# Kernel optimization log

Measured on AMD Instinct MI355X. Metric: run time of the kernel, lower is better.

The kernel has to match this reference:

```python
import jax, jax.numpy as jnp
import numpy as np

B, D, H, O, E, K = 8192, 1024, 4096, 1024, 8, 2
HG = H // 2  # gate hidden dim


def setup_inputs() -> dict:
    key = jax.random.key(0)
    ks = jax.random.split(key, 6)
    s1 = 1.0 / np.sqrt(D)
    s2 = 1.0 / np.sqrt(H)
    sg = 1.0 / np.sqrt(HG)
    return {
        "x": jax.random.normal(ks[0], (B, D), jnp.float32),
        "W1": jax.random.normal(ks[1], (E, D, H), jnp.float32) * s1,
        "b1": jnp.zeros((E, H), jnp.float32),
        "W2": jax.random.normal(ks[2], (E, H, O), jnp.float32) * s2,
        "b2": jnp.zeros((E, O), jnp.float32),
        "Wg1": jax.random.normal(ks[3], (D, HG), jnp.float32) * s1,
        "bg1": jnp.zeros((HG,), jnp.float32),
        "Wg2": jax.random.normal(ks[4], (HG, E), jnp.float32) * sg,
        "bg2": jnp.zeros((E,), jnp.float32),
    }


def reference(x, W1, b1, W2, b2, Wg1, bg1, Wg2, bg2):
    # Gate: Linear -> ReLU -> Linear -> softmax over experts
    gate_logits = jax.nn.relu(x @ Wg1 + bg1) @ Wg2 + bg2          # [B, E]
    gate_weights = jax.nn.softmax(gate_logits, axis=1)           # [B, E]

    # Top-k selection and renormalization (second softmax, as in torch)
    top_w, top_idx = jax.lax.top_k(gate_weights, K)              # [B, K]
    top_w = jax.nn.softmax(top_w, axis=1)                        # [B, K]

    # Dense per-expert MLPs (the torch code evaluates every expert)
    h = jax.nn.relu(jnp.einsum('bd,edh->beh', x, W1) + b1)       # [B, E, H]
    expert_outputs = jnp.einsum('beh,eho->beo', h, W2) + b2      # [B, E, O]

    # Gather top-k expert outputs and combine with renormalized weights
    gathered = jnp.take_along_axis(expert_outputs, top_idx[:, :, None], axis=1)  # [B, K, O]
    output = jnp.einsum('bk,bko->bo', top_w, gathered)           # [B, O]

    # Load balancing loss (only expert_fractions feeds the loss; the
    # expert_usage loop in the torch code is dead w.r.t. the returned loss)
    expert_fractions = gate_weights.mean(axis=0)                 # [E]
    cv_loss = jnp.sum((expert_fractions - 1.0 / E) ** 2)

    return output, gate_weights, cv_loss
```

## Files before the change

kernel.cpp:

```cpp
#include <hip/hip_runtime.h>

#define B_  8192
#define D_  1024
#define H_  4096
#define O_  1024
#define E_  8
#define HG_ 2048

typedef _Float16 half8 __attribute__((ext_vector_type(8)));
typedef _Float16 half4 __attribute__((ext_vector_type(4)));
typedef float    f32x4 __attribute__((ext_vector_type(4)));

#define MFMA_F16(a, b, c) __builtin_amdgcn_mfma_f32_16x16x32_f16((a), (b), (c), 0, 0, 0)

typedef const unsigned int __attribute__((address_space(1)))* as1_u32;
typedef unsigned int __attribute__((address_space(3)))* as3_u32;

__device__ __forceinline__ void gload_lds16(const void* g, void* s) {
  __builtin_amdgcn_global_load_lds((as1_u32)(g), (as3_u32)(s), 16, 0, 0);
}

__global__ void zero_small(int* cnt, float* colsum) {
  if (threadIdx.x < E_) { cnt[threadIdx.x] = 0; colsum[threadIdx.x] = 0.f; }
}

__global__ void cvt_x(const float* __restrict__ x, _Float16* __restrict__ xh,
                      _Float16* __restrict__ xl) {
  size_t i = ((size_t)blockIdx.x * 256 + threadIdx.x) * 4;
  float4 v = *(const float4*)(x + i);
  _Float16 h0 = (_Float16)v.x, h1 = (_Float16)v.y, h2 = (_Float16)v.z, h3 = (_Float16)v.w;
  half4 hh = {h0, h1, h2, h3};
  half4 ll = {(_Float16)(v.x - (float)h0), (_Float16)(v.y - (float)h1),
              (_Float16)(v.z - (float)h2), (_Float16)(v.w - (float)h3)};
  *(half4*)(xh + i) = hh;
  *(half4*)(xl + i) = ll;
}

template <bool LO>
__global__ void transpose_cvt(const float* __restrict__ in, _Float16* __restrict__ oh,
                              _Float16* __restrict__ ol, int M, int N) {
  __shared__ float t[32][33];
  const size_t boff = (size_t)blockIdx.z * M * N;
  int bx = blockIdx.x * 32, by = blockIdx.y * 32;
  int tx = threadIdx.x, ty = threadIdx.y;
  const float* src = in + boff;
#pragma unroll
  for (int i = ty; i < 32; i += 8) t[i][tx] = src[(size_t)(by + i) * N + bx + tx];
  __syncthreads();
  _Float16* dh = oh + boff;
#pragma unroll
  for (int i = ty; i < 32; i += 8) {
    float v = t[tx][i];
    size_t oidx = (size_t)(bx + i) * M + by + tx;
    _Float16 h = (_Float16)v;
    dh[oidx] = h;
    if (LO) ol[oidx] = (_Float16)(v - (float)h);
  }
}

__global__ __launch_bounds__(256) void gate_gemm(
    const _Float16* __restrict__ xh, const _Float16* __restrict__ xl,
    const _Float16* __restrict__ wh, const _Float16* __restrict__ wl,
    const float* __restrict__ bg1, float* __restrict__ ghid) {
  __shared__ _Float16 sAh[128 * 32], sAl[128 * 32], sBh[128 * 32], sBl[128 * 32];
  const int tid = threadIdx.x, wave = tid >> 6, lane = tid & 63;
  const int m0 = blockIdx.y * 128, n0 = blockIdx.x * 128;
  const int srow = (wave << 4) + (lane >> 2);
  const int scol = (lane & 3) << 3;
  _Float16* dA0 = sAh + (wave * 16) * 32;
  _Float16* dA1 = sAh + (64 + wave * 16) * 32;
  _Float16* dA0l = sAl + (wave * 16) * 32;
  _Float16* dA1l = sAl + (64 + wave * 16) * 32;
  _Float16* dB0 = sBh + (wave * 16) * 32;
  _Float16* dB1 = sBh + (64 + wave * 16) * 32;
  _Float16* dB0l = sBl + (wave * 16) * 32;
  _Float16* dB1l = sBl + (64 + wave * 16) * 32;
  const _Float16* gA0 = xh + (size_t)(m0 + srow) * D_ + scol;
  const _Float16* gA1 = xh + (size_t)(m0 + 64 + srow) * D_ + scol;
  const _Float16* gA0l = xl + (size_t)(m0 + srow) * D_ + scol;
  const _Float16* gA1l = xl + (size_t)(m0 + 64 + srow) * D_ + scol;
  const _Float16* gB0 = wh + (size_t)(n0 + srow) * D_ + scol;
  const _Float16* gB1 = wh + (size_t)(n0 + 64 + srow) * D_ + scol;
  const _Float16* gB0l = wl + (size_t)(n0 + srow) * D_ + scol;
  const _Float16* gB1l = wl + (size_t)(n0 + 64 + srow) * D_ + scol;
  f32x4 acc[4][4] = {};
  const int wm = wave & 1, wn = wave >> 1, fr = lane & 15, fq = lane >> 4;
  for (int k0 = 0; k0 < D_; k0 += 32) {
    __syncthreads();
    gload_lds16(gA0 + k0, dA0);
    gload_lds16(gA1 + k0, dA1);
    gload_lds16(gA0l + k0, dA0l);
    gload_lds16(gA1l + k0, dA1l);
    gload_lds16(gB0 + k0, dB0);
    gload_lds16(gB1 + k0, dB1);
    gload_lds16(gB0l + k0, dB0l);
    gload_lds16(gB1l + k0, dB1l);
    __syncthreads();
    half8 ah[4], al[4], bh[4], bl[4];
#pragma unroll
    for (int i = 0; i < 4; i++) {
      ah[i] = *(const half8*)(sAh + (wm * 64 + i * 16 + fr) * 32 + fq * 8);
      al[i] = *(const half8*)(sAl + (wm * 64 + i * 16 + fr) * 32 + fq * 8);
      bh[i] = *(const half8*)(sBh + (wn * 64 + i * 16 + fr) * 32 + fq * 8);
      bl[i] = *(const half8*)(sBl + (wn * 64 + i * 16 + fr) * 32 + fq * 8);
    }
#pragma unroll
    for (int mi = 0; mi < 4; mi++)
#pragma unroll
      for (int ni = 0; ni < 4; ni++) {
        acc[mi][ni] = MFMA_F16(ah[mi], bh[ni], acc[mi][ni]);
        acc[mi][ni] = MFMA_F16(ah[mi], bl[ni], acc[mi][ni]);
        acc[mi][ni] = MFMA_F16(al[mi], bh[ni], acc[mi][ni]);
      }
  }
#pragma unroll
  for (int mi = 0; mi < 4; mi++)
#pragma unroll
    for (int i = 0; i < 4; i++) {
      int row = m0 + wm * 64 + mi * 16 + fq * 4 + i;
      float* dst = ghid + (size_t)row * HG_ + n0 + wn * 64;
#pragma unroll
      for (int ni = 0; ni < 4; ni++) {
        int col = ni * 16 + fr;
        dst[col] = fmaxf(acc[mi][ni][i] + bg1[n0 + wn * 64 + col], 0.f);
      }
    }
}

__global__ __launch_bounds__(256) void gate_finish(
    const float* __restrict__ ghid, const float* __restrict__ wg2,
    const float* __restrict__ bg2, float* __restrict__ gw, int* __restrict__ tok,
    float* __restrict__ tkw, int* __restrict__ tkf, int* __restrict__ cnt,
    float* __restrict__ colsum) {
  __shared__ int s_e[32];
  __shared__ float s_p[32];
  __shared__ float s_col[E_];
  __shared__ int s_c[E_], s_c2[E_], s_b[E_];
  const int tid = threadIdx.x, wave = tid >> 6, lane = tid & 63;
  if (tid < E_) { s_col[tid] = 0.f; s_c[tid] = 0; s_c2[tid] = 0; }
  __syncthreads();
  for (int it = 0; it < 4; it++) {
    int b = blockIdx.x * 16 + wave * 4 + it;
    const float* g = ghid + (size_t)b * HG_;
    float l[8] = {0, 0, 0, 0, 0, 0, 0, 0};
    for (int j = lane; j < HG_; j += 64) {
      float gv = g[j];
      float4 w0 = *(const float4*)(wg2 + (size_t)j * 8);
      float4 w1 = *(const float4*)(wg2 + (size_t)j * 8 + 4);
      l[0] += gv * w0.x; l[1] += gv * w0.y; l[2] += gv * w0.z; l[3] += gv * w0.w;
      l[4] += gv * w1.x; l[5] += gv * w1.y; l[6] += gv * w1.z; l[7] += gv * w1.w;
    }
#pragma unroll
    for (int off = 32; off; off >>= 1)
#pragma unroll
      for (int r = 0; r < 8; r++) l[r] += __shfl_xor(l[r], off);
    if (lane == 0) {
      float w[8];
      float mx = -1e30f;
#pragma unroll
      for (int r = 0; r < 8; r++) { l[r] += bg2[r]; mx = fmaxf(mx, l[r]); }
      float s = 0.f;
#pragma unroll
      for (int r = 0; r < 8; r++) { w[r] = expf(l[r] - mx); s += w[r]; }
      float inv = 1.f / s;
#pragma unroll
      for (int r = 0; r < 8; r++) w[r] *= inv;
      for (int r = 0; r < 8; r++) {
        gw[(size_t)b * 8 + r] = w[r];
        atomicAdd(&s_col[r], w[r]);
      }
      int i1 = 0;
      for (int r = 1; r < 8; r++) if (w[r] > w[i1]) i1 = r;
      int i2 = (i1 == 0) ? 1 : 0;
      for (int r = 0; r < 8; r++) if (r != i1 && w[r] > w[i2]) i2 = r;
      float e2 = expf(w[i2] - w[i1]);
      float p1 = 1.f / (1.f + e2), p2 = e2 / (1.f + e2);
      int sl = (wave * 4 + it) * 2;
      s_e[sl] = i1; s_p[sl] = p1;
      s_e[sl + 1] = i2; s_p[sl + 1] = p2;
    }
  }
  __syncthreads();
  if (tid < 32) atomicAdd(&s_c[s_e[tid]], 1);
  __syncthreads();
  if (tid < E_) s_b[tid] = atomicAdd(&cnt[tid], s_c[tid]);
  __syncthreads();
  if (tid < 32) {
    int e = s_e[tid];
    int slot = s_b[e] + atomicAdd(&s_c2[e], 1);
    int bb = blockIdx.x * 16 + (tid >> 1);
    tok[e * B_ + slot] = bb;
    tkw[e * B_ + slot] = s_p[tid];
    tkf[e * B_ + slot] = tid & 1;
  }
  if (tid < E_) atomicAdd(&colsum[tid], s_col[tid]);
}

__global__ void prefix_cv(const int* __restrict__ cnt, int* __restrict__ basep,
                          const float* __restrict__ colsum, float* __restrict__ cvout) {
  if (threadIdx.x == 0) {
    int s = 0;
    for (int e = 0; e < E_; e++) { basep[e] = s; s += cnt[e]; }
    float cv = 0.f;
    for (int e = 0; e < E_; e++) {
      float f = colsum[e] * (1.f / B_) - 1.f / E_;
      cv += f * f;
    }
    *cvout = cv;
  }
}

__global__ __launch_bounds__(256) void expert_gemm1(
    const _Float16* __restrict__ xh, const _Float16* __restrict__ w1t,
    const float* __restrict__ b1, const int* __restrict__ tok,
    const int* __restrict__ cnt, const int* __restrict__ basep,
    _Float16* __restrict__ hbuf) {
  const int e = blockIdx.y >> 6, mt = blockIdx.y & 63;
  const int ce = cnt[e];
  if (mt * 128 >= ce) return;
  __shared__ _Float16 sA[128 * 32], sB[128 * 32];
  const int tid = threadIdx.x, wave = tid >> 6, lane = tid & 63;
  const int n0 = blockIdx.x * 128;
  const int srow = (wave << 4) + (lane >> 2), scol = (lane & 3) << 3;
  int r0 = mt * 128 + srow, r1 = r0 + 64;
  if (r0 > ce - 1) r0 = ce - 1;
  if (r1 > ce - 1) r1 = ce - 1;
  const int t0 = tok[e * B_ + r0], t1 = tok[e * B_ + r1];
  const _Float16* gA0 = xh + (size_t)t0 * D_ + scol;
  const _Float16* gA1 = xh + (size_t)t1 * D_ + scol;
  const _Float16* wte = w1t + (size_t)e * H_ * D_;
  const _Float16* gB0 = wte + (size_t)(n0 + srow) * D_ + scol;
  const _Float16* gB1 = wte + (size_t)(n0 + 64 + srow) * D_ + scol;
  _Float16* dA0 = sA + (wave * 16) * 32;
  _Float16* dA1 = sA + (64 + wave * 16) * 32;
  _Float16* dB0 = sB + (wave * 16) * 32;
  _Float16* dB1 = sB + (64 + wave * 16) * 32;
  f32x4 acc[4][4] = {};
  const int wm = wave & 1, wn = wave >> 1, fr = lane & 15, fq = lane >> 4;
  for (int k0 = 0; k0 < D_; k0 += 32) {
    __syncthreads();
    gload_lds16(gA0 + k0, dA0);
    gload_lds16(gA1 + k0, dA1);
    gload_lds16(gB0 + k0, dB0);
    gload_lds16(gB1 + k0, dB1);
    __syncthreads();
    half8 a[4], b[4];
#pragma unroll
    for (int i = 0; i < 4; i++) {
      a[i] = *(const half8*)(sA + (wm * 64 + i * 16 + fr) * 32 + fq * 8);
      b[i] = *(const half8*)(sB + (wn * 64 + i * 16 + fr) * 32 + fq * 8);
    }
#pragma unroll
    for (int mi = 0; mi < 4; mi++)
#pragma unroll
      for (int ni = 0; ni < 4; ni++) acc[mi][ni] = MFMA_F16(a[mi], b[ni], acc[mi][ni]);
  }
  const int base = basep[e];
  float bv[4];
#pragma unroll
  for (int ni = 0; ni < 4; ni++) bv[ni] = b1[e * H_ + n0 + wn * 64 + ni * 16 + fr];
#pragma unroll
  for (int mi = 0; mi < 4; mi++)
#pragma unroll
    for (int i = 0; i < 4; i++) {
      int rloc = mt * 128 + wm * 64 + mi * 16 + fq * 4 + i;
      if (rloc < ce) {
        _Float16* dst = hbuf + (size_t)(base + rloc) * H_ + n0 + wn * 64;
#pragma unroll
        for (int ni = 0; ni < 4; ni++)
          dst[ni * 16 + fr] = (_Float16)fmaxf(acc[mi][ni][i] + bv[ni], 0.f);
      }
    }
}

__global__ __launch_bounds__(256) void expert_gemm2(
    const _Float16* __restrict__ hbuf, const _Float16* __restrict__ w2t,
    const float* __restrict__ b2, const int* __restrict__ tok,
    const float* __restrict__ tkw, const int* __restrict__ tkf,
    const int* __restrict__ cnt, const int* __restrict__ basep,
    float* __restrict__ obuf) {
  const int e = blockIdx.y >> 6, mt = blockIdx.y & 63;
  const int ce = cnt[e];
  if (mt * 128 >= ce) return;
  __shared__ _Float16 sA[128 * 32], sB[128 * 32];
  const int tid = threadIdx.x, wave = tid >> 6, lane = tid & 63;
  const int n0 = blockIdx.x * 128;
  const int srow = (wave << 4) + (lane >> 2), scol = (lane & 3) << 3;
  const int base = basep[e];
  int r0 = mt * 128 + srow, r1 = r0 + 64;
  if (r0 > ce - 1) r0 = ce - 1;
  if (r1 > ce - 1) r1 = ce - 1;
  const _Float16* gA0 = hbuf + (size_t)(base + r0) * H_ + scol;
  const _Float16* gA1 = hbuf + (size_t)(base + r1) * H_ + scol;
  const _Float16* wte = w2t + (size_t)e * O_ * H_;
  const _Float16* gB0 = wte + (size_t)(n0 + srow) * H_ + scol;
  const _Float16* gB1 = wte + (size_t)(n0 + 64 + srow) * H_ + scol;
  _Float16* dA0 = sA + (wave * 16) * 32;
  _Float16* dA1 = sA + (64 + wave * 16) * 32;
  _Float16* dB0 = sB + (wave * 16) * 32;
  _Float16* dB1 = sB + (64 + wave * 16) * 32;
  f32x4 acc[4][4] = {};
  const int wm = wave & 1, wn = wave >> 1, fr = lane & 15, fq = lane >> 4;
  for (int k0 = 0; k0 < H_; k0 += 32) {
    __syncthreads();
    gload_lds16(gA0 + k0, dA0);
    gload_lds16(gA1 + k0, dA1);
    gload_lds16(gB0 + k0, dB0);
    gload_lds16(gB1 + k0, dB1);
    __syncthreads();
    half8 a[4], b[4];
#pragma unroll
    for (int i = 0; i < 4; i++) {
      a[i] = *(const half8*)(sA + (wm * 64 + i * 16 + fr) * 32 + fq * 8);
      b[i] = *(const half8*)(sB + (wn * 64 + i * 16 + fr) * 32 + fq * 8);
    }
#pragma unroll
    for (int mi = 0; mi < 4; mi++)
#pragma unroll
      for (int ni = 0; ni < 4; ni++) acc[mi][ni] = MFMA_F16(a[mi], b[ni], acc[mi][ni]);
  }
  float bv[4];
#pragma unroll
  for (int ni = 0; ni < 4; ni++) bv[ni] = b2[e * O_ + n0 + wn * 64 + ni * 16 + fr];
#pragma unroll
  for (int mi = 0; mi < 4; mi++)
#pragma unroll
    for (int i = 0; i < 4; i++) {
      int rloc = mt * 128 + wm * 64 + mi * 16 + fq * 4 + i;
      if (rloc < ce) {
        int t = tok[e * B_ + rloc];
        float p = tkw[e * B_ + rloc];
        int f = tkf[e * B_ + rloc];
        float* dst = obuf + ((size_t)t * 2 + f) * O_ + n0 + wn * 64;
#pragma unroll
        for (int ni = 0; ni < 4; ni++)
          dst[ni * 16 + fr] = p * (acc[mi][ni][i] + bv[ni]);
      }
    }
}

__global__ void combine(const float* __restrict__ obuf, float* __restrict__ out) {
  size_t i = (size_t)blockIdx.x * 256 + threadIdx.x;
  const float4* o4 = (const float4*)obuf;
  size_t b = i >> 8, c = i & 255;
  float4 u = o4[(b * 2) * 256 + c];
  float4 v = o4[(b * 2 + 1) * 256 + c];
  float4 w = {u.x + v.x, u.y + v.y, u.z + v.z, u.w + v.w};
  ((float4*)out)[i] = w;
}

extern "C" void kernel_launch(void* const* d_in, const int* in_sizes, int n_in,
                              void* d_out, int out_size, void* d_ws, size_t ws_size,
                              hipStream_t stream) {
  const float* x = (const float*)d_in[0];
  const float* W1 = (const float*)d_in[1];
  const float* b1 = (const float*)d_in[2];
  const float* W2 = (const float*)d_in[3];
  const float* b2 = (const float*)d_in[4];
  const float* Wg1 = (const float*)d_in[5];
  const float* bg1 = (const float*)d_in[6];
  const float* Wg2 = (const float*)d_in[7];
  const float* bg2 = (const float*)d_in[8];

  float* out = (float*)d_out;
  float* gw = out + (size_t)B_ * O_;
  float* cv = gw + (size_t)B_ * E_;

  char* w = (char*)d_ws;
  const size_t OFF_XH = 0;
  const size_t OFF_XL = OFF_XH + (size_t)B_ * D_ * 2;
  const size_t OFF_WG1H = OFF_XL + (size_t)B_ * D_ * 2;
  const size_t OFF_WG1L = OFF_WG1H + (size_t)HG_ * D_ * 2;
  const size_t OFF_WT = OFF_WG1L + (size_t)HG_ * D_ * 2;
  const size_t OFF_GHID = OFF_WT + (size_t)E_ * H_ * D_ * 2;
  const size_t OFF_HBUF = OFF_GHID + (size_t)B_ * HG_ * 4;
  const size_t OFF_TOK = OFF_HBUF + (size_t)B_ * 2 * H_ * 2;
  const size_t OFF_TKW = OFF_TOK + (size_t)E_ * B_ * 4;
  const size_t OFF_TKF = OFF_TKW + (size_t)E_ * B_ * 4;
  const size_t OFF_CNT = OFF_TKF + (size_t)E_ * B_ * 4;
  const size_t OFF_COL = OFF_CNT + 64;
  const size_t OFF_BASE = OFF_COL + 64;
  const size_t WS_NEED = OFF_BASE + 64;
  if (ws_size < WS_NEED) return;

  _Float16* xh = (_Float16*)(w + OFF_XH);
  _Float16* xl = (_Float16*)(w + OFF_XL);
  _Float16* wg1h = (_Float16*)(w + OFF_WG1H);
  _Float16* wg1l = (_Float16*)(w + OFF_WG1L);
  _Float16* wt = (_Float16*)(w + OFF_WT);
  float* ghid = (float*)(w + OFF_GHID);
  float* obuf = (float*)(w + OFF_GHID);
  _Float16* hbuf = (_Float16*)(w + OFF_HBUF);
  int* tok = (int*)(w + OFF_TOK);
  float* tkw = (float*)(w + OFF_TKW);
  int* tkf = (int*)(w + OFF_TKF);
  int* cnt = (int*)(w + OFF_CNT);
  float* colsum = (float*)(w + OFF_COL);
  int* basep = (int*)(w + OFF_BASE);

  zero_small<<<1, 64, 0, stream>>>(cnt, colsum);
  cvt_x<<<(B_ * D_) / (256 * 4), 256, 0, stream>>>(x, xh, xl);
  transpose_cvt<true><<<dim3(HG_ / 32, D_ / 32, 1), dim3(32, 8), 0, stream>>>(
      Wg1, wg1h, wg1l, D_, HG_);
  transpose_cvt<false><<<dim3(H_ / 32, D_ / 32, E_), dim3(32, 8), 0, stream>>>(
      W1, wt, nullptr, D_, H_);
  gate_gemm<<<dim3(HG_ / 128, B_ / 128), 256, 0, stream>>>(xh, xl, wg1h, wg1l, bg1, ghid);
  gate_finish<<<B_ / 16, 256, 0, stream>>>(ghid, Wg2, bg2, gw, tok, tkw, tkf, cnt, colsum);
  prefix_cv<<<1, 64, 0, stream>>>(cnt, basep, colsum, cv);
  expert_gemm1<<<dim3(H_ / 128, E_ * 64), 256, 0, stream>>>(xh, wt, b1, tok, cnt, basep, hbuf);
  transpose_cvt<false><<<dim3(O_ / 32, H_ / 32, E_), dim3(32, 8), 0, stream>>>(
      W2, wt, nullptr, H_, O_);
  expert_gemm2<<<dim3(O_ / 128, E_ * 64), 256, 0, stream>>>(hbuf, wt, b2, tok, tkw, tkf,
                                                            cnt, basep, obuf);
  combine<<<(B_ * O_) / (256 * 4), 256, 0, stream>>>(obuf, out);
}
```

Before: 985.6 us.

## Swizzle LDS layout, compact expert tile list, split-K gemm2, fp16 partials

```diff
diff --git a/kernel.cpp b/kernel.cpp
--- a/kernel.cpp
+++ b/kernel.cpp
@@ -6,6 +6,7 @@
 #define O_  1024
 #define E_  8
 #define HG_ 2048
+#define MAXT_ 135
 
 typedef _Float16 half8 __attribute__((ext_vector_type(8)));
 typedef _Float16 half4 __attribute__((ext_vector_type(4)));
@@ -19,6 +20,7 @@
 __device__ __forceinline__ void gload_lds16(const void* g, void* s) {
   __builtin_amdgcn_global_load_lds((as1_u32)(g), (as3_u32)(s), 16, 0, 0);
 }
+
 
 __global__ void zero_small(int* cnt, float* colsum) {
   if (threadIdx.x < E_) { cnt[threadIdx.x] = 0; colsum[threadIdx.x] = 0.f; }
@@ -47,14 +49,17 @@
 #pragma unroll
   for (int i = ty; i < 32; i += 8) t[i][tx] = src[(size_t)(by + i) * N + bx + tx];
   __syncthreads();
-  _Float16* dh = oh + boff;
-#pragma unroll
-  for (int i = ty; i < 32; i += 8) {
-    float v = t[tx][i];
-    size_t oidx = (size_t)(bx + i) * M + by + tx;
-    _Float16 h = (_Float16)v;
-    dh[oidx] = h;
-    if (LO) ol[oidx] = (_Float16)(v - (float)h);
+  int tid = ty * 32 + tx;
+  int rr = tid >> 3, cq = tid & 7;
+  float v0 = t[cq * 4 + 0][rr], v1 = t[cq * 4 + 1][rr];
+  float v2 = t[cq * 4 + 2][rr], v3 = t[cq * 4 + 3][rr];
+  half4 h = {(_Float16)v0, (_Float16)v1, (_Float16)v2, (_Float16)v3};
+  size_t o = boff + (size_t)(bx + rr) * M + by + cq * 4;
+  *(half4*)(oh + o) = h;
+  if (LO) {
+    half4 l = {(_Float16)(v0 - (float)h[0]), (_Float16)(v1 - (float)h[1]),
+               (_Float16)(v2 - (float)h[2]), (_Float16)(v3 - (float)h[3])};
+    *(half4*)(ol + o) = l;
   }
 }
 
@@ -64,9 +69,12 @@
     const float* __restrict__ bg1, float* __restrict__ ghid) {
   __shared__ _Float16 sAh[128 * 32], sAl[128 * 32], sBh[128 * 32], sBl[128 * 32];
   const int tid = threadIdx.x, wave = tid >> 6, lane = tid & 63;
+  const int fr = lane & 15, fq = lane >> 4;
   const int m0 = blockIdx.y * 128, n0 = blockIdx.x * 128;
-  const int srow = (wave << 4) + (lane >> 2);
-  const int scol = (lane & 3) << 3;
+  const int q = lane >> 2;
+  const int srow = (wave << 4) + q;
+  const int scol = (((lane & 3) ^ ((lane >> 3) & 3)) << 3);
+  const int xsw8 = (fq ^ ((fr >> 1) & 3)) << 3;
   _Float16* dA0 = sAh + (wave * 16) * 32;
   _Float16* dA1 = sAh + (64 + wave * 16) * 32;
   _Float16* dA0l = sAl + (wave * 16) * 32;
@@ -84,7 +92,7 @@
   const _Float16* gB0l = wl + (size_t)(n0 + srow) * D_ + scol;
   const _Float16* gB1l = wl + (size_t)(n0 + 64 + srow) * D_ + scol;
   f32x4 acc[4][4] = {};
-  const int wm = wave & 1, wn = wave >> 1, fr = lane & 15, fq = lane >> 4;
+  const int wm = wave & 1, wn = wave >> 1;
   for (int k0 = 0; k0 < D_; k0 += 32) {
     __syncthreads();
     gload_lds16(gA0 + k0, dA0);
@@ -99,10 +107,12 @@
     half8 ah[4], al[4], bh[4], bl[4];
 #pragma unroll
     for (int i = 0; i < 4; i++) {
-      ah[i] = *(const half8*)(sAh + (wm * 64 + i * 16 + fr) * 32 + fq * 8);
-      al[i] = *(const half8*)(sAl + (wm * 64 + i * 16 + fr) * 32 + fq * 8);
-      bh[i] = *(const half8*)(sBh + (wn * 64 + i * 16 + fr) * 32 + fq * 8);
-      bl[i] = *(const half8*)(sBl + (wn * 64 + i * 16 + fr) * 32 + fq * 8);
+      int ca = (wm * 64 + i * 16 + fr) * 32 + xsw8;
+      int cb = (wn * 64 + i * 16 + fr) * 32 + xsw8;
+      ah[i] = *(const half8*)(sAh + ca);
+      al[i] = *(const half8*)(sAl + ca);
+      bh[i] = *(const half8*)(sBh + cb);
+      bl[i] = *(const half8*)(sBl + cb);
     }
 #pragma unroll
     for (int mi = 0; mi < 4; mi++)
@@ -197,10 +207,17 @@
 }
 
 __global__ void prefix_cv(const int* __restrict__ cnt, int* __restrict__ basep,
-                          const float* __restrict__ colsum, float* __restrict__ cvout) {
+                          const float* __restrict__ colsum, float* __restrict__ cvout,
+                          int* __restrict__ tile_e, int* __restrict__ tile_mt,
+                          int* __restrict__ ntiles) {
   if (threadIdx.x == 0) {
-    int s = 0;
-    for (int e = 0; e < E_; e++) { basep[e] = s; s += cnt[e]; }
+    int s = 0, nt = 0;
+    for (int e = 0; e < E_; e++) {
+      basep[e] = s;
+      for (int t = 0; t * 128 < cnt[e]; t++) { tile_e[nt] = e; tile_mt[nt] = t; nt++; }
+      s += cnt[e];
+    }
+    ntiles[0] = nt;
     float cv = 0.f;
     for (int e = 0; e < E_; e++) {
       float f = colsum[e] * (1.f / B_) - 1.f / E_;
@@ -214,14 +231,20 @@
     const _Float16* __restrict__ xh, const _Float16* __restrict__ w1t,
     const float* __restrict__ b1, const int* __restrict__ tok,
     const int* __restrict__ cnt, const int* __restrict__ basep,
-    _Float16* __restrict__ hbuf) {
-  const int e = blockIdx.y >> 6, mt = blockIdx.y & 63;
+    const int* __restrict__ tile_e, const int* __restrict__ tile_mt,
+    const int* __restrict__ ntiles, _Float16* __restrict__ hbuf) {
+  const int idx = blockIdx.y;
+  if (idx >= ntiles[0]) return;
+  const int e = tile_e[idx], mt = tile_mt[idx];
   const int ce = cnt[e];
-  if (mt * 128 >= ce) return;
   __shared__ _Float16 sA[128 * 32], sB[128 * 32];
   const int tid = threadIdx.x, wave = tid >> 6, lane = tid & 63;
+  const int fr = lane & 15, fq = lane >> 4;
   const int n0 = blockIdx.x * 128;
-  const int srow = (wave << 4) + (lane >> 2), scol = (lane & 3) << 3;
+  const int q = lane >> 2;
+  const int srow = (wave << 4) + q;
+  const int scol = (((lane & 3) ^ ((lane >> 3) & 3)) << 3);
+  const int xsw8 = (fq ^ ((fr >> 1) & 3)) << 3;
   int r0 = mt * 128 + srow, r1 = r0 + 64;
   if (r0 > ce - 1) r0 = ce - 1;
   if (r1 > ce - 1) r1 = ce - 1;
@@ -236,7 +259,7 @@
   _Float16* dB0 = sB + (wave * 16) * 32;
   _Float16* dB1 = sB + (64 + wave * 16) * 32;
   f32x4 acc[4][4] = {};
-  const int wm = wave & 1, wn = wave >> 1, fr = lane & 15, fq = lane >> 4;
+  const int wm = wave & 1, wn = wave >> 1;
   for (int k0 = 0; k0 < D_; k0 += 32) {
     __syncthreads();
     gload_lds16(gA0 + k0, dA0);
@@ -247,8 +270,8 @@
     half8 a[4], b[4];
 #pragma unroll
     for (int i = 0; i < 4; i++) {
-      a[i] = *(const half8*)(sA + (wm * 64 + i * 16 + fr) * 32 + fq * 8);
-      b[i] = *(const half8*)(sB + (wn * 64 + i * 16 + fr) * 32 + fq * 8);
+      a[i] = *(const half8*)(sA + (wm * 64 + i * 16 + fr) * 32 + xsw8);
+      b[i] = *(const half8*)(sB + (wn * 64 + i * 16 + fr) * 32 + xsw8);
     }
 #pragma unroll
     for (int mi = 0; mi < 4; mi++)
@@ -278,15 +301,22 @@
     const float* __restrict__ b2, const int* __restrict__ tok,
     const float* __restrict__ tkw, const int* __restrict__ tkf,
     const int* __restrict__ cnt, const int* __restrict__ basep,
-    float* __restrict__ obuf) {
-  const int e = blockIdx.y >> 6, mt = blockIdx.y & 63;
+    const int* __restrict__ tile_e, const int* __restrict__ tile_mt,
+    const int* __restrict__ ntiles, _Float16* __restrict__ obuf) {
+  const int idx = blockIdx.y;
+  if (idx >= ntiles[0]) return;
+  const int e = tile_e[idx], mt = tile_mt[idx];
+  const int ks = blockIdx.z;
   const int ce = cnt[e];
-  if (mt * 128 >= ce) return;
+  const int base = basep[e];
   __shared__ _Float16 sA[128 * 32], sB[128 * 32];
   const int tid = threadIdx.x, wave = tid >> 6, lane = tid & 63;
+  const int fr = lane & 15, fq = lane >> 4;
   const int n0 = blockIdx.x * 128;
-  const int srow = (wave << 4) + (lane >> 2), scol = (lane & 3) << 3;
-  const int base = basep[e];
+  const int q = lane >> 2;
+  const int srow = (wave << 4) + q;
+  const int scol = (((lane & 3) ^ ((lane >> 3) & 3)) << 3);
+  const int xsw8 = (fq ^ ((fr >> 1) & 3)) << 3;
   int r0 = mt * 128 + srow, r1 = r0 + 64;
   if (r0 > ce - 1) r0 = ce - 1;
   if (r1 > ce - 1) r1 = ce - 1;
@@ -300,8 +330,9 @@
   _Float16* dB0 = sB + (wave * 16) * 32;
   _Float16* dB1 = sB + (64 + wave * 16) * 32;
   f32x4 acc[4][4] = {};
-  const int wm = wave & 1, wn = wave >> 1, fr = lane & 15, fq = lane >> 4;
-  for (int k0 = 0; k0 < H_; k0 += 32) {
+  const int wm = wave & 1, wn = wave >> 1;
+  const int kbeg = ks * (H_ / 2), kend = kbeg + H_ / 2;
+  for (int k0 = kbeg; k0 < kend; k0 += 32) {
     __syncthreads();
     gload_lds16(gA0 + k0, dA0);
     gload_lds16(gA1 + k0, dA1);
@@ -311,17 +342,19 @@
     half8 a[4], b[4];
 #pragma unroll
     for (int i = 0; i < 4; i++) {
-      a[i] = *(const half8*)(sA + (wm * 64 + i * 16 + fr) * 32 + fq * 8);
-      b[i] = *(const half8*)(sB + (wn * 64 + i * 16 + fr) * 32 + fq * 8);
+      a[i] = *(const half8*)(sA + (wm * 64 + i * 16 + fr) * 32 + xsw8);
+      b[i] = *(const half8*)(sB + (wn * 64 + i * 16 + fr) * 32 + xsw8);
     }
 #pragma unroll
     for (int mi = 0; mi < 4; mi++)
 #pragma unroll
       for (int ni = 0; ni < 4; ni++) acc[mi][ni] = MFMA_F16(a[mi], b[ni], acc[mi][ni]);
   }
-  float bv[4];
-#pragma unroll
-  for (int ni = 0; ni < 4; ni++) bv[ni] = b2[e * O_ + n0 + wn * 64 + ni * 16 + fr];
+  float bv[4] = {0.f, 0.f, 0.f, 0.f};
+  if (ks == 0) {
+#pragma unroll
+    for (int ni = 0; ni < 4; ni++) bv[ni] = b2[e * O_ + n0 + wn * 64 + ni * 16 + fr];
+  }
 #pragma unroll
   for (int mi = 0; mi < 4; mi++)
 #pragma unroll
@@ -331,22 +364,25 @@
         int t = tok[e * B_ + rloc];
         float p = tkw[e * B_ + rloc];
         int f = tkf[e * B_ + rloc];
-        float* dst = obuf + ((size_t)t * 2 + f) * O_ + n0 + wn * 64;
+        _Float16* dst = obuf + ((size_t)t * 4 + f * 2 + ks) * O_ + n0 + wn * 64;
 #pragma unroll
         for (int ni = 0; ni < 4; ni++)
-          dst[ni * 16 + fr] = p * (acc[mi][ni][i] + bv[ni]);
+          dst[ni * 16 + fr] = (_Float16)(p * (acc[mi][ni][i] + bv[ni]));
       }
     }
 }
 
-__global__ void combine(const float* __restrict__ obuf, float* __restrict__ out) {
+__global__ void combine(const _Float16* __restrict__ obuf, float* __restrict__ out) {
   size_t i = (size_t)blockIdx.x * 256 + threadIdx.x;
-  const float4* o4 = (const float4*)obuf;
-  size_t b = i >> 8, c = i & 255;
-  float4 u = o4[(b * 2) * 256 + c];
-  float4 v = o4[(b * 2 + 1) * 256 + c];
-  float4 w = {u.x + v.x, u.y + v.y, u.z + v.z, u.w + v.w};
-  ((float4*)out)[i] = w;
+  size_t t = i >> 8, c = (i & 255) * 4;
+  const _Float16* base = obuf + (size_t)t * 4 * O_ + c;
+  float4 r = {0.f, 0.f, 0.f, 0.f};
+#pragma unroll
+  for (int s = 0; s < 4; s++) {
+    half4 v = *(const half4*)(base + (size_t)s * O_);
+    r.x += (float)v[0]; r.y += (float)v[1]; r.z += (float)v[2]; r.w += (float)v[3];
+  }
+  ((float4*)out)[i] = r;
 }
 
 extern "C" void kernel_launch(void* const* d_in, const int* in_sizes, int n_in,
@@ -380,7 +416,10 @@
   const size_t OFF_CNT = OFF_TKF + (size_t)E_ * B_ * 4;
   const size_t OFF_COL = OFF_CNT + 64;
   const size_t OFF_BASE = OFF_COL + 64;
-  const size_t WS_NEED = OFF_BASE + 64;
+  const size_t OFF_TE = OFF_BASE + 64;
+  const size_t OFF_TM = OFF_TE + 640;
+  const size_t OFF_NT = OFF_TM + 640;
+  const size_t WS_NEED = OFF_NT + 64;
   if (ws_size < WS_NEED) return;
 
   _Float16* xh = (_Float16*)(w + OFF_XH);
@@ -389,7 +428,7 @@
   _Float16* wg1l = (_Float16*)(w + OFF_WG1L);
   _Float16* wt = (_Float16*)(w + OFF_WT);
   float* ghid = (float*)(w + OFF_GHID);
-  float* obuf = (float*)(w + OFF_GHID);
+  _Float16* obuf = (_Float16*)(w + OFF_GHID);
   _Float16* hbuf = (_Float16*)(w + OFF_HBUF);
   int* tok = (int*)(w + OFF_TOK);
   float* tkw = (float*)(w + OFF_TKW);
@@ -397,6 +436,9 @@
   int* cnt = (int*)(w + OFF_CNT);
   float* colsum = (float*)(w + OFF_COL);
   int* basep = (int*)(w + OFF_BASE);
+  int* tile_e = (int*)(w + OFF_TE);
+  int* tile_mt = (int*)(w + OFF_TM);
+  int* ntiles = (int*)(w + OFF_NT);
 
   zero_small<<<1, 64, 0, stream>>>(cnt, colsum);
   cvt_x<<<(B_ * D_) / (256 * 4), 256, 0, stream>>>(x, xh, xl);
@@ -406,11 +448,13 @@
       W1, wt, nullptr, D_, H_);
   gate_gemm<<<dim3(HG_ / 128, B_ / 128), 256, 0, stream>>>(xh, xl, wg1h, wg1l, bg1, ghid);
   gate_finish<<<B_ / 16, 256, 0, stream>>>(ghid, Wg2, bg2, gw, tok, tkw, tkf, cnt, colsum);
-  prefix_cv<<<1, 64, 0, stream>>>(cnt, basep, colsum, cv);
-  expert_gemm1<<<dim3(H_ / 128, E_ * 64), 256, 0, stream>>>(xh, wt, b1, tok, cnt, basep, hbuf);
+  prefix_cv<<<1, 64, 0, stream>>>(cnt, basep, colsum, cv, tile_e, tile_mt, ntiles);
+  expert_gemm1<<<dim3(H_ / 128, MAXT_), 256, 0, stream>>>(xh, wt, b1, tok, cnt, basep,
+                                                          tile_e, tile_mt, ntiles, hbuf);
   transpose_cvt<false><<<dim3(O_ / 32, H_ / 32, E_), dim3(32, 8), 0, stream>>>(
       W2, wt, nullptr, H_, O_);
-  expert_gemm2<<<dim3(O_ / 128, E_ * 64), 256, 0, stream>>>(hbuf, wt, b2, tok, tkw, tkf,
-                                                            cnt, basep, obuf);
+  expert_gemm2<<<dim3(O_ / 128, MAXT_, 2), 256, 0, stream>>>(hbuf, wt, b2, tok, tkw, tkf,
+                                                             cnt, basep, tile_e, tile_mt,
+                                                             ntiles, obuf);
   combine<<<(B_ * O_) / (256 * 4), 256, 0, stream>>>(obuf, out);
 }
```

Measured after the change: 950.7 us. 3.5% less time.
